# Optimization experiments

Measured on AMD Instinct MI355X. Metric: run time of the kernel, lower is better.

The kernel has to match this reference:

```python
import jax, jax.numpy as jnp
import numpy as np

B, N, H, HD = 32, 256, 6, 32            # windows, tokens/window (16x16), heads, head_dim
C = H * HD                               # dim = 192
TOPK_IN, TOPK_OUT = 64, 32               # incoming pfa topk, num_topk[layer_id]
NBIAS = (2 * 16 - 1) ** 2                # relative-position bias table size = 961
SCALE = HD ** -0.5
EPS = 1e-20


def setup_inputs() -> dict:
    key = jax.random.key(0)
    ks = jax.random.split(key, 7)
    qkvp = jax.random.normal(ks[0], (B, N, 4 * C), dtype=jnp.float32)
    pfa_values = jax.random.uniform(ks[1], (B, H, N, TOPK_IN), dtype=jnp.float32)
    pfa_index = jax.random.randint(ks[2], (B, H, N, TOPK_IN), 0, N, dtype=jnp.int64)
    rpi = jax.random.randint(ks[3], (N, N), 0, NBIAS, dtype=jnp.int64)
    rpb_table = 0.02 * jax.random.normal(ks[4], (NBIAS, H), dtype=jnp.float32)
    proj_w = 0.02 * jax.random.normal(ks[5], (C, C), dtype=jnp.float32)
    proj_b = jnp.zeros((C,), dtype=jnp.float32)
    return {"qkvp": qkvp, "pfa_values": pfa_values, "pfa_index": pfa_index,
            "rpi": rpi, "rpb_table": rpb_table, "proj_w": proj_w, "proj_b": proj_b}


def _gather_rows(x, idx):
    # x: [b, h, n, d], idx: [b, h, n, t] -> [b, h, n, t, d] = x[b, h, idx[b,h,n,t], :]
    return jnp.take_along_axis(x[:, :, None, :, :], idx[..., None], axis=3)


def reference(qkvp, pfa_values, pfa_index, rpi, rpb_table, proj_w, proj_b):
    b_, n, c4 = qkvp.shape
    c = c4 // 4
    hd = c // H
    qkvp = qkvp.reshape(b_, n, 4, H, hd).transpose(2, 0, 3, 1, 4)  # [4, b, h, n, hd]
    q, k, v, v_lepe = qkvp[0], qkvp[1], qkvp[2], qkvp[3]
    q = q * SCALE

    # sparse QK^T over gathered keys: attn[b,h,i,t] = <q[b,h,i], k[b,h,idx[b,h,i,t]]>
    k_sel = _gather_rows(k, pfa_index)                      # [b, h, n, TOPK_IN, hd]
    attn = jnp.einsum('bhnd,bhntd->bhnt', q, k_sel)

    # relative position bias, gathered along the sparse key index
    rpb = rpb_table[rpi.reshape(-1)].reshape(n, n, H).transpose(2, 0, 1)  # [h, n, n]
    bias = jnp.take_along_axis(jnp.broadcast_to(rpb[None], (b_, H, n, n)),
                               pfa_index, axis=-1)           # [b, h, n, TOPK_IN]
    attn = attn + bias

    attn = jax.nn.softmax(attn, axis=-1)

    # progressive focusing: modulate by previous attn values and renormalize
    attn = attn * pfa_values
    denom = attn.sum(axis=-1, keepdims=True)
    attn = (attn + EPS) / (denom + EPS)

    # prune to self.topk = TOPK_OUT entries and remap indices
    topv, topi = jax.lax.top_k(attn, TOPK_OUT)               # [b, h, n, TOPK_OUT]
    new_index = jnp.take_along_axis(pfa_index, topi, axis=-1)

    # sparse attn @ V over gathered values, plus LePE residual
    v_sel = _gather_rows(v, new_index)                       # [b, h, n, TOPK_OUT, hd]
    x = jnp.einsum('bhnt,bhntd->bhnd', topv, v_sel) + v_lepe
    x = x.transpose(0, 2, 1, 3).reshape(b_, n, c)
    x = x @ proj_w.T + proj_b
    return x, topv, new_index
```

## Files before the change

kernel.cpp:

```cpp
#include <hip/hip_runtime.h>

#define B_    32
#define N_    256
#define H_    6
#define HD_   32
#define C_    192
#define C4_   768
#define TKIN  64
#define TKOUT 32
#define WULP  32u

__global__ __launch_bounds__(128) void attn_topk_kernel(
    const float* __restrict__ qkvp,
    const float* __restrict__ pfa_values,
    const int*   __restrict__ pfa_index,
    const int*   __restrict__ rpi,
    const float* __restrict__ rpb_table,
    float* __restrict__ x_pre,
    float* __restrict__ out_topv,
    float* __restrict__ out_nidx)
{
    const int lane  = threadIdx.x & 63;
    const int wslot = threadIdx.x >> 6;

    const int n  = blockIdx.x;
    const int x  = n & 7;
    const int r  = n >> 3;
    const int bq = r / 768;
    const int wb = r - bq * 768;
    const int b  = x * 4 + bq;
    const int row = b * (H_ * N_) + wb * 2 + wslot;

    const int rem = row - b * (H_ * N_);
    const int h   = rem / N_;
    const int i   = rem - h * N_;

    const int row_off = row * TKIN;
    const int idx  = pfa_index[row_off + lane];
    const float pv = pfa_values[row_off + lane];

    __shared__ __align__(16) uint2 s_pk[2][64];
    __shared__ float  s_k32x[2][64];
    __shared__ double s_k64[2][64];
    __shared__ uint2  s_ai[2][TKOUT];

    const float* qp = qkvp + (size_t)(b * N_ + i) * C4_ + h * HD_;
    const float* kp = qkvp + (size_t)(b * N_ + idx) * C4_ + C_ + h * HD_;
    const float bias = rpb_table[rpi[i * N_ + idx] * H_ + h];

    float acc;
    {
        #pragma clang fp contract(off)
        const float SC = 0.17677669529663687f;
        acc = 0.f;
        #pragma unroll
        for (int d0 = 0; d0 < 8; ++d0) {
            const float4 k4 = *(const float4*)(kp + 4 * d0);
            const float* k4p = (const float*)&k4;
            #pragma unroll
            for (int t = 0; t < 4; ++t) {
                const float qd   = qp[4 * d0 + t] * SC;
                const float prod = qd * k4p[t];
                acc = acc + prod;
            }
        }
        acc = acc + bias;
    }

    float m = acc;
    #pragma unroll
    for (int s = 32; s; s >>= 1) m = fmaxf(m, __shfl_xor(m, s));

    float e;
    {
        #pragma clang fp contract(off)
        const float t = acc - m;
        e = (float)exp((double)t);
    }

    float ssum;
    {
        #pragma clang fp contract(off)
        float y = e, r2 = e;
        #pragma unroll
        for (int k = 1; k < 8; ++k) { y = __shfl_down(y, 8); r2 = r2 + y; }
        const float t1 = r2 + __shfl_xor(r2, 1);
        const float t2 = t1 + __shfl_xor(t1, 2);
        const float t3 = t2 + __shfl_xor(t2, 4);
        ssum = __shfl(t3, 0);
    }

    float w;
    {
        #pragma clang fp contract(off)
        const float s32 = e / ssum;
        w = s32 * pv;
    }

    float denom;
    {
        #pragma clang fp contract(off)
        float y = w, r2 = w;
        #pragma unroll
        for (int k = 1; k < 8; ++k) { y = __shfl_down(y, 8); r2 = r2 + y; }
        const float t1 = r2 + __shfl_xor(r2, 1);
        const float t2 = t1 + __shfl_xor(t1, 2);
        const float t3 = t2 + __shfl_xor(t2, 4);
        denom = __shfl(t3, 0);
    }

    float a32;
    {
        #pragma clang fp contract(off)
        a32 = (w + 1e-20f) / (denom + 1e-20f);
    }

    const unsigned abits = __float_as_uint(a32);
    const unsigned long long myK =
        ((unsigned long long)abits << 6) | (unsigned long long)(63 - lane);
    s_pk[wslot][lane] = make_uint2((unsigned)myK, (unsigned)(myK >> 32));

    int rank = 0;
    #pragma unroll
    for (int j2 = 0; j2 < 32; ++j2) {
        const uint4 kk = *(const uint4*)&s_pk[wslot][j2 * 2];
        const unsigned long long K0 =
            ((unsigned long long)kk.y << 32) | (unsigned long long)kk.x;
        const unsigned long long K1 =
            ((unsigned long long)kk.w << 32) | (unsigned long long)kk.z;
        rank += (K0 > myK);
        rank += (K1 > myK);
    }

    {
        const int sorted = __builtin_amdgcn_ds_permute(rank << 2, (int)abits);
        const int nxt    = __shfl_down(sorted, 1);
        const unsigned gap = (unsigned)sorted - (unsigned)nxt;
        const bool nearf = (lane < 63) && (gap <= WULP);
        if (__any(nearf)) {
            double acc64 = 0.0;
            #pragma unroll
            for (int d0 = 0; d0 < 8; ++d0) {
                const float4 q4 = *(const float4*)(qp + 4 * d0);
                const float4 k4 = *(const float4*)(kp + 4 * d0);
                acc64 = fma((double)q4.x, (double)k4.x, acc64);
                acc64 = fma((double)q4.y, (double)k4.y, acc64);
                acc64 = fma((double)q4.z, (double)k4.z, acc64);
                acc64 = fma((double)q4.w, (double)k4.w, acc64);
            }
            acc64 = acc64 * 0.17677669529663687 + (double)bias;
            const double okey = exp(acc64) * (double)pv;
            s_k64[wslot][lane] = okey;
            s_k32x[wslot][lane] = a32;

            rank = 0;
            #pragma unroll
            for (int j = 0; j < 64; ++j) {
                const float  kj32 = s_k32x[wslot][j];
                const double kj64 = s_k64[wslot][j];
                const bool tie  = (kj32 == a32);
                const bool lt64 = (kj64 < okey);
                const bool gt64 = (kj64 > okey);
                const bool eq64 = (kj64 == okey);
                const bool before = tie ? (lt64 || (eq64 && j < lane))
                                        : (gt64 || (eq64 && kj32 > a32));
                rank += before;
            }
        }
    }

    if (rank < TKOUT) {
        const size_t obase = (size_t)row * TKOUT + rank;
        out_topv[obase] = a32;
        out_nidx[obase] = (float)idx;
        s_ai[wslot][rank] = make_uint2(abits, (unsigned)idx);
    }

    const int d    = lane & 31;
    const int half = lane >> 5;
    float xd = 0.f;
    #pragma unroll
    for (int s16 = 0; s16 < 16; ++s16) {
        const int sI = half * 16 + s16;
        const uint2 ai = s_ai[wslot][sI];
        const float av = __uint_as_float(ai.x);
        const int   vi = (int)ai.y;
        xd += av * qkvp[(size_t)(b * N_ + vi) * C4_ + 2 * C_ + h * HD_ + d];
    }
    xd += __shfl_xor(xd, 32);
    if (half == 0) {
        const float lepe = qkvp[(size_t)(b * N_ + i) * C4_ + 3 * C_ + h * HD_ + d];
        x_pre[(size_t)(b * N_ + i) * C_ + h * HD_ + d] = xd + lepe;
    }
}

#define TB_ 8
__global__ __launch_bounds__(192) void proj_kernel(
    const float* __restrict__ x_pre,
    const float* __restrict__ w,
    const float* __restrict__ bias,
    float* __restrict__ out)
{
    __shared__ float xs[TB_ * C_];
    const int o    = threadIdx.x;
    const int tok0 = blockIdx.x * TB_;

    #pragma unroll
    for (int r = 0; r < TB_; ++r)
        xs[r * C_ + o] = x_pre[(size_t)(tok0 + r) * C_ + o];
    __syncthreads();

    float accv[TB_];
    #pragma unroll
    for (int t = 0; t < TB_; ++t) accv[t] = 0.f;

    const float* wrow = w + (size_t)o * C_;
    for (int c = 0; c < C_; c += 4) {
        const float4 wv = *(const float4*)(wrow + c);
        #pragma unroll
        for (int t = 0; t < TB_; ++t) {
            const float4 xv = *(const float4*)(&xs[t * C_ + c]);
            accv[t] += xv.x * wv.x + xv.y * wv.y + xv.z * wv.z + xv.w * wv.w;
        }
    }
    const float bo = bias[o];
    #pragma unroll
    for (int t = 0; t < TB_; ++t)
        out[(size_t)(tok0 + t) * C_ + o] = accv[t] + bo;
}

extern "C" void kernel_launch(void* const* d_in, const int* in_sizes, int n_in,
                              void* d_out, int out_size, void* d_ws, size_t ws_size,
                              hipStream_t stream) {
    const float* qkvp       = (const float*)d_in[0];
    const float* pfa_values = (const float*)d_in[1];
    const int*   pfa_index  = (const int*)d_in[2];
    const int*   rpi        = (const int*)d_in[3];
    const float* rpb_table  = (const float*)d_in[4];
    const float* proj_w     = (const float*)d_in[5];
    const float* proj_b     = (const float*)d_in[6];

    float* out = (float*)d_out;
    float* out_x    = out;
    float* out_topv = out + (size_t)B_ * N_ * C_;
    float* out_nidx = out_topv + (size_t)B_ * H_ * N_ * TKOUT;

    float* x_pre = (float*)d_ws;

    const int rows = B_ * H_ * N_;
    attn_topk_kernel<<<rows / 2, 128, 0, stream>>>(
        qkvp, pfa_values, pfa_index, rpi, rpb_table, x_pre, out_topv, out_nidx);

    const int ntok = B_ * N_;
    proj_kernel<<<ntok / TB_, 192, 0, stream>>>(x_pre, proj_w, proj_b, out_x);
}
```

Measured before the change: 112.1 us.

## Stage per-head K tile in shared memory and loop rows per block

Each block now loads the whole 256x32 K slice for one (window, head) into padded shared memory, then loops its 8 waves over 64 query rows, reading gathered keys from LDS instead of global memory. This removes repeated scattered global K loads across rows that share the same head. In exchange it uses larger blocks, a grid of only 768 blocks, about 34KB+ of LDS per block, and scalar strided LDS reads that may bank-conflict. An unused GAP32 define is also added.

```diff
diff --git a/kernel.cpp b/kernel.cpp
--- a/kernel.cpp
+++ b/kernel.cpp
@@ -8,9 +8,10 @@
 #define C4_   768
 #define TKIN  64
 #define TKOUT 32
+#define GAP32 4u
 #define WULP  32u
 
-__global__ __launch_bounds__(128) void attn_topk_kernel(
+__global__ __launch_bounds__(512) void attn_topk_kernel(
     const float* __restrict__ qkvp,
     const float* __restrict__ pfa_values,
     const int*   __restrict__ pfa_index,
@@ -22,175 +23,181 @@
 {
     const int lane  = threadIdx.x & 63;
     const int wslot = threadIdx.x >> 6;
+    const int tid   = threadIdx.x;
 
     const int n  = blockIdx.x;
     const int x  = n & 7;
     const int r  = n >> 3;
-    const int bq = r / 768;
-    const int wb = r - bq * 768;
-    const int b  = x * 4 + bq;
-    const int row = b * (H_ * N_) + wb * 2 + wslot;
-
-    const int rem = row - b * (H_ * N_);
-    const int h   = rem / N_;
-    const int i   = rem - h * N_;
-
-    const int row_off = row * TKIN;
-    const int idx  = pfa_index[row_off + lane];
-    const float pv = pfa_values[row_off + lane];
-
-    __shared__ __align__(16) uint2 s_pk[2][64];
-    __shared__ float  s_k32x[2][64];
-    __shared__ double s_k64[2][64];
-    __shared__ uint2  s_ai[2][TKOUT];
-
-    const float* qp = qkvp + (size_t)(b * N_ + i) * C4_ + h * HD_;
-    const float* kp = qkvp + (size_t)(b * N_ + idx) * C4_ + C_ + h * HD_;
-    const float bias = rpb_table[rpi[i * N_ + idx] * H_ + h];
-
-    float acc;
+    const int b  = x * 4 + r / 24;
+    const int rr = r % 24;
+    const int h  = rr >> 2;
+    const int quarter = rr & 3;
+
+    __shared__ float  Kl[256][33];
+    __shared__ __align__(16) uint2 s_pk[8][64];
+    __shared__ float  s_k32x[8][64];
+    __shared__ double s_k64[8][64];
+    __shared__ uint2  s_ai[8][TKOUT];
+
     {
-        #pragma clang fp contract(off)
-        const float SC = 0.17677669529663687f;
-        acc = 0.f;
-        #pragma unroll
-        for (int d0 = 0; d0 < 8; ++d0) {
-            const float4 k4 = *(const float4*)(kp + 4 * d0);
-            const float* k4p = (const float*)&k4;
-            #pragma unroll
-            for (int t = 0; t < 4; ++t) {
-                const float qd   = qp[4 * d0 + t] * SC;
-                const float prod = qd * k4p[t];
+        #pragma unroll
+        for (int c = 0; c < 4; ++c) {
+            const int elem = c * 512 + tid;
+            const int krow = elem >> 3;
+            const int kcol = (elem & 7) * 4;
+            const float4 v = *(const float4*)(
+                qkvp + (size_t)(b * N_ + krow) * C4_ + C_ + h * HD_ + kcol);
+            Kl[krow][kcol + 0] = v.x;
+            Kl[krow][kcol + 1] = v.y;
+            Kl[krow][kcol + 2] = v.z;
+            Kl[krow][kcol + 3] = v.w;
+        }
+    }
+    __syncthreads();
+
+    for (int it = 0; it < 8; ++it) {
+        const int i   = quarter * 64 + it * 8 + wslot;
+        const int row = (b * H_ + h) * N_ + i;
+
+        const int row_off = row * TKIN;
+        const int idx  = pfa_index[row_off + lane];
+        const float pv = pfa_values[row_off + lane];
+
+        const float* qp = qkvp + (size_t)(b * N_ + i) * C4_ + h * HD_;
+        const float bias = rpb_table[rpi[i * N_ + idx] * H_ + h];
+        const float* kl = &Kl[idx][0];
+
+        float acc;
+        {
+            #pragma clang fp contract(off)
+            const float SC = 0.17677669529663687f;
+            acc = 0.f;
+            for (int d = 0; d < HD_; ++d) {
+                const float qd   = qp[d] * SC;
+                const float prod = qd * kl[d];
                 acc = acc + prod;
             }
-        }
-        acc = acc + bias;
-    }
-
-    float m = acc;
-    #pragma unroll
-    for (int s = 32; s; s >>= 1) m = fmaxf(m, __shfl_xor(m, s));
-
-    float e;
-    {
-        #pragma clang fp contract(off)
-        const float t = acc - m;
-        e = (float)exp((double)t);
-    }
-
-    float ssum;
-    {
-        #pragma clang fp contract(off)
-        float y = e, r2 = e;
-        #pragma unroll
-        for (int k = 1; k < 8; ++k) { y = __shfl_down(y, 8); r2 = r2 + y; }
-        const float t1 = r2 + __shfl_xor(r2, 1);
-        const float t2 = t1 + __shfl_xor(t1, 2);
-        const float t3 = t2 + __shfl_xor(t2, 4);
-        ssum = __shfl(t3, 0);
-    }
-
-    float w;
-    {
-        #pragma clang fp contract(off)
-        const float s32 = e / ssum;
-        w = s32 * pv;
-    }
-
-    float denom;
-    {
-        #pragma clang fp contract(off)
-        float y = w, r2 = w;
-        #pragma unroll
-        for (int k = 1; k < 8; ++k) { y = __shfl_down(y, 8); r2 = r2 + y; }
-        const float t1 = r2 + __shfl_xor(r2, 1);
-        const float t2 = t1 + __shfl_xor(t1, 2);
-        const float t3 = t2 + __shfl_xor(t2, 4);
-        denom = __shfl(t3, 0);
-    }
-
-    float a32;
-    {
-        #pragma clang fp contract(off)
-        a32 = (w + 1e-20f) / (denom + 1e-20f);
-    }
-
-    const unsigned abits = __float_as_uint(a32);
-    const unsigned long long myK =
-        ((unsigned long long)abits << 6) | (unsigned long long)(63 - lane);
-    s_pk[wslot][lane] = make_uint2((unsigned)myK, (unsigned)(myK >> 32));
-
-    int rank = 0;
-    #pragma unroll
-    for (int j2 = 0; j2 < 32; ++j2) {
-        const uint4 kk = *(const uint4*)&s_pk[wslot][j2 * 2];
-        const unsigned long long K0 =
-            ((unsigned long long)kk.y << 32) | (unsigned long long)kk.x;
-        const unsigned long long K1 =
-            ((unsigned long long)kk.w << 32) | (unsigned long long)kk.z;
-        rank += (K0 > myK);
-        rank += (K1 > myK);
-    }
-
-    {
-        const int sorted = __builtin_amdgcn_ds_permute(rank << 2, (int)abits);
-        const int nxt    = __shfl_down(sorted, 1);
-        const unsigned gap = (unsigned)sorted - (unsigned)nxt;
-        const bool nearf = (lane < 63) && (gap <= WULP);
-        if (__any(nearf)) {
-            double acc64 = 0.0;
+            acc = acc + bias;
+        }
+
+        float m = acc;
+        #pragma unroll
+        for (int s = 32; s; s >>= 1) m = fmaxf(m, __shfl_xor(m, s));
+
+        float e;
+        {
+            #pragma clang fp contract(off)
+            const float t = acc - m;
+            e = (float)exp((double)t);
+        }
+
+        float ssum;
+        {
+            #pragma clang fp contract(off)
+            float y = e, r2 = e;
             #pragma unroll
-            for (int d0 = 0; d0 < 8; ++d0) {
-                const float4 q4 = *(const float4*)(qp + 4 * d0);
-                const float4 k4 = *(const float4*)(kp + 4 * d0);
-                acc64 = fma((double)q4.x, (double)k4.x, acc64);
-                acc64 = fma((double)q4.y, (double)k4.y, acc64);
-                acc64 = fma((double)q4.z, (double)k4.z, acc64);
-                acc64 = fma((double)q4.w, (double)k4.w, acc64);
+            for (int k = 1; k < 8; ++k) { y = __shfl_down(y, 8); r2 = r2 + y; }
+            const float t1 = r2 + __shfl_xor(r2, 1);
+            const float t2 = t1 + __shfl_xor(t1, 2);
+            const float t3 = t2 + __shfl_xor(t2, 4);
+            ssum = __shfl(t3, 0);
+        }
+
+        float w;
+        {
+            #pragma clang fp contract(off)
+            const float s32 = e / ssum;
+            w = s32 * pv;
+        }
+
+        float denom;
+        {
+            #pragma clang fp contract(off)
+            float y = w, r2 = w;
+            #pragma unroll
+            for (int k = 1; k < 8; ++k) { y = __shfl_down(y, 8); r2 = r2 + y; }
+            const float t1 = r2 + __shfl_xor(r2, 1);
+            const float t2 = t1 + __shfl_xor(t1, 2);
+            const float t3 = t2 + __shfl_xor(t2, 4);
+            denom = __shfl(t3, 0);
+        }
+
+        float a32;
+        {
+            #pragma clang fp contract(off)
+            a32 = (w + 1e-20f) / (denom + 1e-20f);
+        }
+
+        const unsigned abits = __float_as_uint(a32);
+        const unsigned long long myK =
+            ((unsigned long long)abits << 6) | (unsigned long long)(63 - lane);
+        s_pk[wslot][lane] = make_uint2((unsigned)myK, (unsigned)(myK >> 32));
+
+        int rank = 0;
+        #pragma unroll
+        for (int j2 = 0; j2 < 32; ++j2) {
+            const uint4 kk = *(const uint4*)&s_pk[wslot][j2 * 2];
+            const unsigned long long K0 =
+                ((unsigned long long)kk.y << 32) | (unsigned long long)kk.x;
+            const unsigned long long K1 =
+                ((unsigned long long)kk.w << 32) | (unsigned long long)kk.z;
+            rank += (K0 > myK);
+            rank += (K1 > myK);
+        }
+
+        {
+            const int sorted = __builtin_amdgcn_ds_permute(rank << 2, (int)abits);
+            const int nxt    = __shfl_down(sorted, 1);
+            const unsigned gap = (unsigned)sorted - (unsigned)nxt;
+            const bool nearf = (lane < 63) && (gap <= WULP);
+            if (__any(nearf)) {
+                double acc64 = 0.0;
+                for (int d = 0; d < HD_; ++d)
+                    acc64 = fma((double)qp[d], (double)kl[d], acc64);
+                acc64 = acc64 * 0.17677669529663687 + (double)bias;
+                const double okey = exp(acc64) * (double)pv;
+                s_k64[wslot][lane] = okey;
+                s_k32x[wslot][lane] = a32;
+
+                rank = 0;
+                #pragma unroll
+                for (int j = 0; j < 64; ++j) {
+                    const float  kj32 = s_k32x[wslot][j];
+                    const double kj64 = s_k64[wslot][j];
+                    const bool tie  = (kj32 == a32);
+                    const bool lt64 = (kj64 < okey);
+                    const bool gt64 = (kj64 > okey);
+                    const bool eq64 = (kj64 == okey);
+                    const bool before = tie ? (lt64 || (eq64 && j < lane))
+                                            : (gt64 || (eq64 && kj32 > a32));
+                    rank += before;
+                }
             }
-            acc64 = acc64 * 0.17677669529663687 + (double)bias;
-            const double okey = exp(acc64) * (double)pv;
-            s_k64[wslot][lane] = okey;
-            s_k32x[wslot][lane] = a32;
-
-            rank = 0;
-            #pragma unroll
-            for (int j = 0; j < 64; ++j) {
-                const float  kj32 = s_k32x[wslot][j];
-                const double kj64 = s_k64[wslot][j];
-                const bool tie  = (kj32 == a32);
-                const bool lt64 = (kj64 < okey);
-                const bool gt64 = (kj64 > okey);
-                const bool eq64 = (kj64 == okey);
-                const bool before = tie ? (lt64 || (eq64 && j < lane))
-                                        : (gt64 || (eq64 && kj32 > a32));
-                rank += before;
-            }
-        }
-    }
-
-    if (rank < TKOUT) {
-        const size_t obase = (size_t)row * TKOUT + rank;
-        out_topv[obase] = a32;
-        out_nidx[obase] = (float)idx;
-        s_ai[wslot][rank] = make_uint2(abits, (unsigned)idx);
-    }
-
-    const int d    = lane & 31;
-    const int half = lane >> 5;
-    float xd = 0.f;
-    #pragma unroll
-    for (int s16 = 0; s16 < 16; ++s16) {
-        const int sI = half * 16 + s16;
-        const uint2 ai = s_ai[wslot][sI];
-        const float av = __uint_as_float(ai.x);
-        const int   vi = (int)ai.y;
-        xd += av * qkvp[(size_t)(b * N_ + vi) * C4_ + 2 * C_ + h * HD_ + d];
-    }
-    xd += __shfl_xor(xd, 32);
-    if (half == 0) {
-        const float lepe = qkvp[(size_t)(b * N_ + i) * C4_ + 3 * C_ + h * HD_ + d];
-        x_pre[(size_t)(b * N_ + i) * C_ + h * HD_ + d] = xd + lepe;
+        }
+
+        if (rank < TKOUT) {
+            const size_t obase = (size_t)row * TKOUT + rank;
+            out_topv[obase] = a32;
+            out_nidx[obase] = (float)idx;
+            s_ai[wslot][rank] = make_uint2(abits, (unsigned)idx);
+        }
+
+        const int d    = lane & 31;
+        const int half = lane >> 5;
+        float xd = 0.f;
+        #pragma unroll
+        for (int s16 = 0; s16 < 16; ++s16) {
+            const int sI = half * 16 + s16;
+            const uint2 ai = s_ai[wslot][sI];
+            const float av = __uint_as_float(ai.x);
+            const int   vi = (int)ai.y;
+            xd += av * qkvp[(size_t)(b * N_ + vi) * C4_ + 2 * C_ + h * HD_ + d];
+        }
+        xd += __shfl_xor(xd, 32);
+        if (half == 0) {
+            const float lepe = qkvp[(size_t)(b * N_ + i) * C4_ + 3 * C_ + h * HD_ + d];
+            x_pre[(size_t)(b * N_ + i) * C_ + h * HD_ + d] = xd + lepe;
+        }
     }
 }
 
@@ -247,8 +254,7 @@
 
     float* x_pre = (float*)d_ws;
 
-    const int rows = B_ * H_ * N_;
-    attn_topk_kernel<<<rows / 2, 128, 0, stream>>>(
+    attn_topk_kernel<<<768, 512, 0, stream>>>(
         qkvp, pfa_values, pfa_index, rpi, rpb_table, x_pre, out_topv, out_nidx);
 
     const int ntok = B_ * N_;
```

New measurement: 110.3 us. About the same (-1.6%).
